# Kernel tuning notes

Hardware: AMD Instinct MI355X
Metric: run time of the kernel (lower is better)

## Reference

```python
import jax, jax.numpy as jnp
import numpy as np

HEADS = 4
HEAD_DIM = 32
DIM = 256
EPS = 1e-12  # F.normalize eps


def setup_inputs() -> dict:
    key = jax.random.key(0)
    ks = jax.random.split(key, 5)
    inner = HEADS * HEAD_DIM
    x = jax.random.normal(ks[0], (4, DIM, 64, 64), dtype=jnp.float32)
    g = jax.random.normal(ks[1], (DIM,), dtype=jnp.float32) * 0.02 + 1.0  # RMSNorm gain
    w_qkv = jax.random.normal(ks[2], (3 * inner, DIM), dtype=jnp.float32) * (DIM ** -0.5)
    w_out = jax.random.normal(ks[3], (DIM, inner), dtype=jnp.float32) * (inner ** -0.5)
    b_out = jax.random.normal(ks[4], (DIM,), dtype=jnp.float32) * 0.01
    return {"x": x, "g": g, "w_qkv": w_qkv, "w_out": w_out, "b_out": b_out}


def reference(x, g, w_qkv, w_out, b_out):
    b, c, h, w = x.shape
    n = h * w
    # RMSNorm over channel dim: F.normalize(x, dim=1) * g * sqrt(dim)
    xn = x * jax.lax.rsqrt(jnp.mean(x * x, axis=1, keepdims=True) + EPS) * g[None, :, None, None]
    # 1x1 conv QKV (no bias): [b, 3*heads*head_dim, h, w]
    qkv = jnp.einsum('bchw,oc->bohw', xn, w_qkv)
    q, k, v = jnp.split(qkv, 3, axis=1)

    def to_bhnd(t):
        # [b, heads*head_dim, h, w] -> [b, heads, n, head_dim]
        return t.reshape(b, HEADS, HEAD_DIM, n).transpose(0, 1, 3, 2)

    q, k, v = to_bhnd(q), to_bhnd(k), to_bhnd(v)
    scale = HEAD_DIM ** -0.5
    sim = jnp.einsum('bhid,bhjd->bhij', q, k) * scale  # [b, heads, n, n]
    attn = jax.nn.softmax(sim, axis=-1)
    out = jnp.einsum('bhij,bhjd->bhid', attn, v)  # [b, heads, n, head_dim]
    # [b, heads, n, head_dim] -> [b, heads*head_dim, h, w]
    out = out.transpose(0, 1, 3, 2).reshape(b, HEADS * HEAD_DIM, h, w)
    # 1x1 conv output projection with bias
    return jnp.einsum('bchw,oc->bohw', out, w_out) + b_out[None, :, None, None]
```

## Files before the change

### kernel.cpp

```cpp
#include <hip/hip_runtime.h>
#include <hip/hip_bf16.h>
#include <stdint.h>
#include <stddef.h>

typedef __attribute__((ext_vector_type(8))) short short8;
typedef __attribute__((ext_vector_type(4))) float f32x4;
typedef __attribute__((ext_vector_type(16))) float f32x16;
typedef __attribute__((ext_vector_type(4))) unsigned int uint4v;

#define MFMA16(a, b, c) __builtin_amdgcn_mfma_f32_16x16x32_bf16((a), (b), (c), 0, 0, 0)
#define MFMA32(a, b, c) __builtin_amdgcn_mfma_f32_32x32x16_bf16((a), (b), (c), 0, 0, 0)

__device__ __forceinline__ unsigned short f2bf(float f) {
  unsigned int u = __builtin_bit_cast(unsigned int, f);
  u += 0x7fffu + ((u >> 16) & 1u);
  return (unsigned short)(u >> 16);
}

__device__ __forceinline__ unsigned int pk2(float lo, float hi) {
  return (unsigned int)f2bf(lo) | ((unsigned int)f2bf(hi) << 16);
}

__device__ __forceinline__ unsigned int pkc(float lo, float hi) {
  __hip_bfloat162 h = __float22bfloat162_rn(make_float2(lo, hi));
  unsigned int u;
  __builtin_memcpy(&u, &h, 4);
  return u;
}

__device__ __forceinline__ short8 mk8(const unsigned short* p) {
  return *(const short8*)p;
}

__device__ __forceinline__ float redsum32(float v) {
  return v + __shfl_xor(v, 32);
}

__device__ __forceinline__ f32x16 zero16() {
  f32x16 v;
#pragma unroll
  for (int i = 0; i < 16; ++i) v[i] = 0.f;
  return v;
}

__device__ __forceinline__ int swz40(int row, int c) {
  return row * 40 + ((((c >> 3) ^ (row >> 3)) & 3) << 3) + (c & 7);
}

__global__ __launch_bounds__(256) void k_prep(const float* __restrict__ wq,
                                              const float* __restrict__ wo,
                                              unsigned short* __restrict__ wq_bf,
                                              unsigned short* __restrict__ wo_bf) {
  int i = blockIdx.x * 256 + threadIdx.x;
  if (i < 98304) wq_bf[i] = f2bf(wq[i]);
  if (i < 32768) wo_bf[i] = f2bf(wo[i]);
}

__global__ __launch_bounds__(256) void k_qkv(const float* __restrict__ x,
                                             const float* __restrict__ g,
                                             const unsigned short* __restrict__ wq_bf,
                                             unsigned short* __restrict__ qbuf,
                                             unsigned short* __restrict__ kbuf,
                                             unsigned short* __restrict__ vbuf) {
  int bid = blockIdx.x;
  int b = bid / 384;
  int rem = bid % 384;
  int ot = rem / 64;
  int pt = rem % 64;
  int o0 = ot * 64, p0 = pt * 64;

  __shared__ unsigned short xnT[2][64 * 40];
  __shared__ float sqv[16][64];
  __shared__ float rl[64];

  int t = threadIdx.x;
  int lane = t & 63, w = t >> 6;
  int lr = lane & 15, lg = lane >> 4;
  int pq = t & 15;
  int cpg = t >> 4;

  const float* xb = x + (size_t)b * 256 * 4096;
  const unsigned short* wqrow = wq_bf + (size_t)(o0 + w * 16 + lr) * 256;

  f32x4 acc[4];
  f32x4 z = {0.f, 0.f, 0.f, 0.f};
#pragma unroll
  for (int i = 0; i < 4; ++i) acc[i] = z;
  f32x4 sacc = z;

#define STAGE_CHUNK(buf, c0)                                                   \
  {                                                                            \
    int cb = (c0) + cpg * 2;                                                   \
    f32x4 xa = *(const f32x4*)&xb[(size_t)cb * 4096 + p0 + pq * 4];            \
    f32x4 xc = *(const f32x4*)&xb[(size_t)(cb + 1) * 4096 + p0 + pq * 4];      \
    float ga = g[cb], gc = g[cb + 1];                                          \
    int cloc = cpg * 2;                                                        \
    _Pragma("unroll")                                                          \
    for (int k = 0; k < 4; ++k) {                                              \
      sacc[k] += xa[k] * xa[k] + xc[k] * xc[k];                                \
      *(unsigned int*)&xnT[buf][swz40(pq * 4 + k, cloc)] =                     \
          pkc(xa[k] * ga, xc[k] * gc);                                         \
    }                                                                          \
  }

  STAGE_CHUNK(0, 0)
  __syncthreads();

  for (int cc = 0; cc < 8; ++cc) {
    int cur = cc & 1;
    if (cc < 7) STAGE_CHUNK(cur ^ 1, (cc + 1) * 32)
    short8 af = mk8(wqrow + cc * 32 + lg * 8);
#pragma unroll
    for (int pt16 = 0; pt16 < 4; ++pt16) {
      short8 bf = mk8(&xnT[cur][swz40(pt16 * 16 + lr, lg * 8)]);
      acc[pt16] = MFMA16(af, bf, acc[pt16]);
    }
    __syncthreads();
  }
#undef STAGE_CHUNK

#pragma unroll
  for (int k = 0; k < 4; ++k) sqv[cpg][pq * 4 + k] = sacc[k];
  __syncthreads();
  if (t < 64) {
    float tot = 0.f;
#pragma unroll
    for (int r = 0; r < 16; ++r) tot += sqv[r][t];
    rl[t] = rsqrtf(tot * (1.0f / 256.0f) + 1e-12f);
  }
  __syncthreads();

  const float cexp = 0.25505654427102996f;
  int obase = o0 + w * 16 + lg * 4;
  if (obase < 128) {
    int h = obase >> 5, d0 = obase & 31;
    unsigned short* dst = qbuf + ((size_t)(b * 4 + h) * 4096) * 32;
#pragma unroll
    for (int pt16 = 0; pt16 < 4; ++pt16) {
      int p = p0 + pt16 * 16 + lr;
      float rr = rl[pt16 * 16 + lr];
      unsigned int u0 = pk2(acc[pt16][0] * rr, acc[pt16][1] * rr);
      unsigned int u1 = pk2(acc[pt16][2] * rr, acc[pt16][3] * rr);
      uint2 uu = {u0, u1};
      *(uint2*)(dst + (size_t)p * 32 + d0) = uu;
    }
  } else if (obase < 256) {
    int oh = obase - 128;
    int h = oh >> 5, d0 = oh & 31;
    int frag = d0 >> 4, hi = (d0 >> 3) & 1, i0 = d0 & 7;
    unsigned short* dst = kbuf + (size_t)(b * 4 + h) * 131072
                         + frag * 512 + hi * 256 + i0;
#pragma unroll
    for (int pt16 = 0; pt16 < 4; ++pt16) {
      int jj = p0 + pt16 * 16 + lr;
      float rr = rl[pt16 * 16 + lr] * cexp;
      int jtile = jj >> 5, j31 = jj & 31;
      uint2 uu = {pk2(acc[pt16][0] * rr, acc[pt16][1] * rr),
                  pk2(acc[pt16][2] * rr, acc[pt16][3] * rr)};
      *(uint2*)(dst + (size_t)jtile * 1024 + j31 * 8) = uu;
    }
  } else {
    int oh = obase - 256;
    int h = oh >> 5, d0 = oh & 31;
    unsigned short* dst = vbuf + (size_t)(b * 4 + h) * 131072;
    int sl = (lr & 3) | ((lr & 4) << 1) | ((lr & 8) >> 1);
#pragma unroll
    for (int pt16 = 0; pt16 < 4; ++pt16) {
      int jj = p0 + pt16 * 16 + sl;
      float rr = rl[pt16 * 16 + lr];
      int jtile = jj >> 5, j5 = jj & 31;
      int frag = j5 >> 4, hi = (j5 >> 3) & 1, i = j5 & 7;
      size_t base = (size_t)jtile * 1024 + frag * 512 + hi * 256 + i;
#pragma unroll
      for (int r = 0; r < 4; ++r)
        dst[base + (d0 + r) * 8] = f2bf(acc[pt16][r] * rr);
    }
  }
}

__global__ __launch_bounds__(256, 5) void k_attn(const unsigned short* __restrict__ qbuf,
                                                 const unsigned short* __restrict__ kbuf,
                                                 const unsigned short* __restrict__ vbuf,
                                                 unsigned short* __restrict__ attno) {
  __shared__ float Ol[3][16][64];
  __shared__ float Ll[3][64];

  int bid = blockIdx.x;
  int wid = ((bid & 7) << 8) | (bid >> 3);
  int qg = wid & 127, bh = wid >> 7;
  int t = threadIdx.x, lane = t & 63, jq = t >> 6;
  int l31 = lane & 31, hi = lane >> 5;

  const unsigned short* qgp = qbuf + (size_t)bh * 4096 * 32;
  const unsigned short* kt = kbuf + (size_t)bh * 131072;
  const unsigned short* vt = vbuf + (size_t)bh * 131072;

  int qrow = qg * 32 + l31;
  short8 qf0 = mk8(qgp + (size_t)qrow * 32 + hi * 8);
  short8 qf1 = mk8(qgp + (size_t)qrow * 32 + 16 + hi * 8);

  const f32x16 z16 = zero16();
  f32x16 oacc = zero16();
  float lsum = 0.f;

  unsigned int koff = (unsigned int)(jq * 32) * 1024u + (unsigned int)lane * 8u;

  short8 kf0 = mk8(kt + koff), kf1 = mk8(kt + koff + 512);
  short8 vf0 = mk8(vt + koff), vf1 = mk8(vt + koff + 512);

  for (int it = 0; it < 32; ++it) {
    __builtin_amdgcn_s_setprio(1);
    f32x16 s = MFMA32(kf0, qf0, z16);
    s = MFMA32(kf1, qf1, s);
    __builtin_amdgcn_s_setprio(0);

    koff += 1024;
    kf0 = mk8(kt + koff);
    kf1 = mk8(kt + koff + 512);

    float p[16];
#pragma unroll
    for (int i = 0; i < 16; ++i) p[i] = __builtin_amdgcn_exp2f(s[i]);

    float s0 = ((p[0] + p[1]) + (p[2] + p[3])) + ((p[4] + p[5]) + (p[6] + p[7]));
    float s1 = ((p[8] + p[9]) + (p[10] + p[11])) + ((p[12] + p[13]) + (p[14] + p[15]));
    lsum += s0 + s1;

    uint4v u0 = {pkc(p[0], p[1]), pkc(p[2], p[3]), pkc(p[4], p[5]), pkc(p[6], p[7])};
    uint4v u1 = {pkc(p[8], p[9]), pkc(p[10], p[11]), pkc(p[12], p[13]), pkc(p[14], p[15])};
    short8 pf0 = __builtin_bit_cast(short8, u0);
    short8 pf1 = __builtin_bit_cast(short8, u1);

    __builtin_amdgcn_s_setprio(1);
    oacc = MFMA32(vf0, pf0, oacc);
    oacc = MFMA32(vf1, pf1, oacc);
    __builtin_amdgcn_s_setprio(0);

    vf0 = mk8(vt + koff);
    vf1 = mk8(vt + koff + 512);
  }

  lsum = redsum32(lsum);

  if (jq > 0) {
#pragma unroll
    for (int i = 0; i < 16; ++i) Ol[jq - 1][i][lane] = oacc[i];
    Ll[jq - 1][lane] = lsum;
  }
  __syncthreads();
  if (jq == 0) {
    float rinv = 1.0f / (lsum + Ll[0][lane] + Ll[1][lane] + Ll[2][lane]);

    int b = bh >> 2, h = bh & 3;
    unsigned short* ob = attno + ((size_t)b * 4096 + qrow) * 128 + h * 32;
#pragma unroll
    for (int r2 = 0; r2 < 8; ++r2) {
      int reg = r2 * 2;
      int dv = (reg & 3) + 8 * (reg >> 2) + 4 * hi;
      float v0 = (oacc[reg] + Ol[0][reg][lane] + Ol[1][reg][lane] + Ol[2][reg][lane]) * rinv;
      float v1 = (oacc[reg + 1] + Ol[0][reg + 1][lane] + Ol[1][reg + 1][lane] + Ol[2][reg + 1][lane]) * rinv;
      *(unsigned int*)(ob + dv) = pk2(v0, v1);
    }
  }
}

__global__ __launch_bounds__(256) void k_out(const unsigned short* __restrict__ attno,
                                             const unsigned short* __restrict__ wo_bf,
                                             const float* __restrict__ bo,
                                             float* __restrict__ out) {
  int bid = blockIdx.x;
  int b = bid >> 8;
  int rem = bid & 255;
  int cog = rem >> 6;
  int p0 = (rem & 63) * 64;
  int co0 = cog * 64;
  int t = threadIdx.x, lane = t & 63, w = t >> 6;
  int lr = lane & 15, lg = lane >> 4;

  f32x4 z = {0.f, 0.f, 0.f, 0.f};
  f32x4 acc[4];
#pragma unroll
  for (int j = 0; j < 4; ++j) acc[j] = z;

  for (int c0 = 0; c0 < 128; c0 += 32) {
    short8 afr = mk8(wo_bf + (size_t)(co0 + w * 16 + lr) * 128 + c0 + lg * 8);
#pragma unroll
    for (int pt16 = 0; pt16 < 4; ++pt16) {
      short8 bfr = mk8(attno + (size_t)(b * 4096 + p0 + pt16 * 16 + lr) * 128 + c0 + lg * 8);
      acc[pt16] = MFMA16(afr, bfr, acc[pt16]);
    }
  }

#pragma unroll
  for (int pt16 = 0; pt16 < 4; ++pt16) {
#pragma unroll
    for (int r = 0; r < 4; ++r) {
      int co = co0 + w * 16 + lg * 4 + r;
      int p = p0 + pt16 * 16 + lr;
      out[((size_t)b * 256 + co) * 4096 + p] = acc[pt16][r] + bo[co];
    }
  }
}

extern "C" void kernel_launch(void* const* d_in, const int* in_sizes, int n_in,
                              void* d_out, int out_size, void* d_ws, size_t ws_size,
                              hipStream_t stream) {
  const float* x = (const float*)d_in[0];
  const float* g = (const float*)d_in[1];
  const float* wq = (const float*)d_in[2];
  const float* wo = (const float*)d_in[3];
  const float* bo = (const float*)d_in[4];
  float* out = (float*)d_out;

  char* ws = (char*)d_ws;
  unsigned short* wq_bf = (unsigned short*)(ws + 65536);
  unsigned short* wo_bf = (unsigned short*)(ws + 262144);
  unsigned short* qbuf = (unsigned short*)(ws + 327680);
  unsigned short* kbuf = (unsigned short*)(ws + 4521984);
  unsigned short* vbuf = (unsigned short*)(ws + 8716288);
  unsigned short* attno = (unsigned short*)(ws + 12910592);

  k_prep<<<dim3(384), dim3(256), 0, stream>>>(wq, wo, wq_bf, wo_bf);
  k_qkv<<<dim3(1536), dim3(256), 0, stream>>>(x, g, wq_bf, qbuf, kbuf, vbuf);
  k_attn<<<dim3(2048), dim3(256), 0, stream>>>(qbuf, kbuf, vbuf, attno);
  k_out<<<dim3(1024), dim3(256), 0, stream>>>(attno, wo_bf, bo, out);
}
```

Before: 97.81 us.

## Store weights and attention output in MFMA fragment-order layouts for coalesced loads

The prep kernel now writes the bf16 QKV and output-projection weights in a layout where each wave's MFMA A-fragment is contiguous. The attention kernel writes its output in the fragment order that k_out consumes directly. Each lane's 16-byte operand load then lands in one contiguous 1KB wave access instead of being strided by row. The cost is more complex index math in the prep and attention epilogue, and attention-output stores that are scattered in 4-byte pieces.

Result: faster. 88.08 us (median of 2 runs) (-9.9%).

```diff
diff --git a/kernel.cpp b/kernel.cpp
--- a/kernel.cpp
+++ b/kernel.cpp
@@ -49,16 +49,26 @@
 
 __global__ __launch_bounds__(256) void k_prep(const float* __restrict__ wq,
                                               const float* __restrict__ wo,
-                                              unsigned short* __restrict__ wq_bf,
-                                              unsigned short* __restrict__ wo_bf) {
+                                              unsigned short* __restrict__ wq_fl,
+                                              unsigned short* __restrict__ wo_fl) {
   int i = blockIdx.x * 256 + threadIdx.x;
-  if (i < 98304) wq_bf[i] = f2bf(wq[i]);
-  if (i < 32768) wo_bf[i] = f2bf(wo[i]);
+  if (i < 98304) {
+    int slot = i & 7, lane = (i >> 3) & 63, cch = (i >> 9) & 7, otile = i >> 12;
+    int o = otile * 16 + (lane & 15);
+    int c = cch * 32 + ((lane >> 4) & 3) * 8 + slot;
+    wq_fl[i] = f2bf(wq[o * 256 + c]);
+  }
+  if (i < 32768) {
+    int slot = i & 7, lane = (i >> 3) & 63, cch = (i >> 9) & 3, cotile = i >> 11;
+    int co = cotile * 16 + (lane & 15);
+    int c = cch * 32 + (lane >> 4) * 8 + slot;
+    wo_fl[i] = f2bf(wo[co * 128 + c]);
+  }
 }
 
 __global__ __launch_bounds__(256) void k_qkv(const float* __restrict__ x,
                                              const float* __restrict__ g,
-                                             const unsigned short* __restrict__ wq_bf,
+                                             const unsigned short* __restrict__ wq_fl,
                                              unsigned short* __restrict__ qbuf,
                                              unsigned short* __restrict__ kbuf,
                                              unsigned short* __restrict__ vbuf) {
@@ -80,7 +90,7 @@
   int cpg = t >> 4;
 
   const float* xb = x + (size_t)b * 256 * 4096;
-  const unsigned short* wqrow = wq_bf + (size_t)(o0 + w * 16 + lr) * 256;
+  const unsigned short* wqf = wq_fl + (size_t)(ot * 4 + w) * 4096 + lane * 8;
 
   f32x4 acc[4];
   f32x4 z = {0.f, 0.f, 0.f, 0.f};
@@ -109,7 +119,7 @@
   for (int cc = 0; cc < 8; ++cc) {
     int cur = cc & 1;
     if (cc < 7) STAGE_CHUNK(cur ^ 1, (cc + 1) * 32)
-    short8 af = mk8(wqrow + cc * 32 + lg * 8);
+    short8 af = mk8(wqf + cc * 512);
 #pragma unroll
     for (int pt16 = 0; pt16 < 4; ++pt16) {
       short8 bf = mk8(&xnT[cur][swz40(pt16 * 16 + lr, lg * 8)]);
@@ -252,20 +262,21 @@
     float rinv = 1.0f / (lsum + Ll[0][lane] + Ll[1][lane] + Ll[2][lane]);
 
     int b = bh >> 2, h = bh & 3;
-    unsigned short* ob = attno + ((size_t)b * 4096 + qrow) * 128 + h * 32;
+    unsigned short* ob = attno + (((size_t)(b * 256 + (qrow >> 4)) * 4 + h) * 512)
+                         + (qrow & 15) * 8;
 #pragma unroll
     for (int r2 = 0; r2 < 8; ++r2) {
       int reg = r2 * 2;
       int dv = (reg & 3) + 8 * (reg >> 2) + 4 * hi;
       float v0 = (oacc[reg] + Ol[0][reg][lane] + Ol[1][reg][lane] + Ol[2][reg][lane]) * rinv;
       float v1 = (oacc[reg + 1] + Ol[0][reg + 1][lane] + Ol[1][reg + 1][lane] + Ol[2][reg + 1][lane]) * rinv;
-      *(unsigned int*)(ob + dv) = pk2(v0, v1);
+      *(unsigned int*)(ob + (dv >> 3) * 128 + (dv & 7)) = pk2(v0, v1);
     }
   }
 }
 
 __global__ __launch_bounds__(256) void k_out(const unsigned short* __restrict__ attno,
-                                             const unsigned short* __restrict__ wo_bf,
+                                             const unsigned short* __restrict__ wo_fl,
                                              const float* __restrict__ bo,
                                              float* __restrict__ out) {
   int bid = blockIdx.x;
@@ -282,11 +293,15 @@
 #pragma unroll
   for (int j = 0; j < 4; ++j) acc[j] = z;
 
-  for (int c0 = 0; c0 < 128; c0 += 32) {
-    short8 afr = mk8(wo_bf + (size_t)(co0 + w * 16 + lr) * 128 + c0 + lg * 8);
-#pragma unroll
-    for (int pt16 = 0; pt16 < 4; ++pt16) {
-      short8 bfr = mk8(attno + (size_t)(b * 4096 + p0 + pt16 * 16 + lr) * 128 + c0 + lg * 8);
+  const unsigned short* wof = wo_fl + (size_t)(cog * 4 + w) * 2048 + lane * 8;
+  const unsigned short* atf = attno + (size_t)(b * 256 + (p0 >> 4)) * 2048 + lane * 8;
+
+#pragma unroll
+  for (int cch = 0; cch < 4; ++cch) {
+    short8 afr = mk8(wof + cch * 512);
+#pragma unroll
+    for (int pt16 = 0; pt16 < 4; ++pt16) {
+      short8 bfr = mk8(atf + (size_t)pt16 * 2048 + cch * 512);
       acc[pt16] = MFMA16(afr, bfr, acc[pt16]);
     }
   }
@@ -313,15 +328,15 @@
   float* out = (float*)d_out;
 
   char* ws = (char*)d_ws;
-  unsigned short* wq_bf = (unsigned short*)(ws + 65536);
-  unsigned short* wo_bf = (unsigned short*)(ws + 262144);
+  unsigned short* wq_fl = (unsigned short*)(ws + 65536);
+  unsigned short* wo_fl = (unsigned short*)(ws + 262144);
   unsigned short* qbuf = (unsigned short*)(ws + 327680);
   unsigned short* kbuf = (unsigned short*)(ws + 4521984);
   unsigned short* vbuf = (unsigned short*)(ws + 8716288);
   unsigned short* attno = (unsigned short*)(ws + 12910592);
 
-  k_prep<<<dim3(384), dim3(256), 0, stream>>>(wq, wo, wq_bf, wo_bf);
-  k_qkv<<<dim3(1536), dim3(256), 0, stream>>>(x, g, wq_bf, qbuf, kbuf, vbuf);
+  k_prep<<<dim3(384), dim3(256), 0, stream>>>(wq, wo, wq_fl, wo_fl);
+  k_qkv<<<dim3(1536), dim3(256), 0, stream>>>(x, g, wq_fl, qbuf, kbuf, vbuf);
   k_attn<<<dim3(2048), dim3(256), 0, stream>>>(qbuf, kbuf, vbuf, attno);
-  k_out<<<dim3(1024), dim3(256), 0, stream>>>(attno, wo_bf, bo, out);
-}
+  k_out<<<dim3(1024), dim3(256), 0, stream>>>(attno, wo_fl, bo, out);
+}
```
